# Kernel optimization log

Measured on AMD Instinct MI355X. Metric: run time of the kernel, lower is better.

## Reference

```python
import jax, jax.numpy as jnp
import numpy as np

OUT, IN, GS = 16384, 4096, 16
G = OUT * IN // GS  # 4194304 groups


def setup_inputs() -> dict:
    key = jax.random.key(0)
    k1, k2, k3, k4 = jax.random.split(key, 4)
    x = jax.random.normal(k1, (8, 32, IN), dtype=jnp.float32)
    weight_q2 = jax.random.randint(k2, (G, GS // 4), 0, 256, dtype=jnp.int32)
    weight_norm = jax.random.uniform(k3, (G, 1), dtype=jnp.float16)
    bias = jax.random.normal(k4, (OUT,), dtype=jnp.float32)
    return {"x": x, "weight_q2": weight_q2, "weight_norm": weight_norm, "bias": bias}


def _dequant_2bit(weight_q2, weight_norm):
    # torch: xq_out[:, i::4] = (xq >> 2i) & 3  =>  element index within group = i + 4*k
    # where k = packed column (slow, stride 4), i = shift index (fast).
    norm = weight_norm.astype(jnp.float32)                      # [G, 1]
    shifts = jnp.arange(4, dtype=jnp.int32) * 2                 # [4]
    vals = (weight_q2[:, :, None] >> shifts) & 3                # [G, 4(pack k), 4(shift i)]
    xq_out = vals.astype(jnp.float32).reshape(G, GS)            # [G, 16], layout k*4 + i
    w = (xq_out / 3.0) * (2.0 * norm) - norm                    # [G, 16]
    return w.reshape(OUT, IN)


def reference(x, weight_q2, weight_norm, bias):
    w = _dequant_2bit(weight_q2, weight_norm)                   # [OUT, IN] fp32
    return jnp.einsum('bsi,oi->bso', x, w) + bias
```

## Files before the change

### kernel.cpp

```cpp
#include <hip/hip_runtime.h>
#include <stdint.h>

#define M_DIM 256
#define N_DIM 16384
#define K_DIM 4096
#define BN 64
#define BK 64
#define NT (K_DIM / BK)

typedef __bf16 bf16x8 __attribute__((ext_vector_type(8)));
typedef float  f32x4  __attribute__((ext_vector_type(4)));

__device__ __forceinline__ uint32_t f2bf(float f) {
  uint32_t u = __float_as_uint(f);
  return (u + 0x7fffu + ((u >> 16) & 1u)) >> 16;
}

#define LDS_BARRIER() \
  asm volatile("s_waitcnt lgkmcnt(0)\n\ts_barrier" ::: "memory")

__global__ __launch_bounds__(256) void cvt_x_kernel(const float* __restrict__ x,
                                                    uint4* __restrict__ ws) {
  int T = blockIdx.x * 256 + threadIdx.x;
  int mb_glob = T >> 13;
  int r       = T & 8191;
  int kch     = r >> 6;
  int L       = r & 63;
  int row = mb_glob * 16 + (L & 15);
  int k   = kch * 32 + (L >> 4) * 8;
  const float* p = x + (size_t)row * K_DIM + k;
  float4 a = *(const float4*)p;
  float4 b = *(const float4*)(p + 4);
  uint4 o;
  o.x = f2bf(a.x) | (f2bf(a.y) << 16);
  o.y = f2bf(a.z) | (f2bf(a.w) << 16);
  o.z = f2bf(b.x) | (f2bf(b.y) << 16);
  o.w = f2bf(b.z) | (f2bf(b.w) << 16);
  ws[T] = o;
}

__device__ __forceinline__ uint4 deq8(uint2 q, float nv) {
  float a2 = nv * (2.0f / 3.0f);
  uint32_t tlo = f2bf(-nv) | (f2bf(fmaf(1.0f, a2, -nv)) << 16);
  uint32_t thi = f2bf(fmaf(2.0f, a2, -nv)) | (f2bf(fmaf(3.0f, a2, -nv)) << 16);
  uint32_t s0 = ((q.x & 3u) | ((q.x & 0xCu) << 14)) * 0x0202u + 0x01000100u;
  uint32_t s1 = (((q.x >> 4) & 3u) | ((q.x & 0xC0u) << 10)) * 0x0202u + 0x01000100u;
  uint32_t s2 = ((q.y & 3u) | ((q.y & 0xCu) << 14)) * 0x0202u + 0x01000100u;
  uint32_t s3 = (((q.y >> 4) & 3u) | ((q.y & 0xC0u) << 10)) * 0x0202u + 0x01000100u;
  uint4 r;
  r.x = __builtin_amdgcn_perm(thi, tlo, s0);
  r.y = __builtin_amdgcn_perm(thi, tlo, s1);
  r.z = __builtin_amdgcn_perm(thi, tlo, s2);
  r.w = __builtin_amdgcn_perm(thi, tlo, s3);
  return r;
}

__global__ __launch_bounds__(512, 4) void gemm2bit_kernel(
    const uint4*    __restrict__ aws,
    const uint32_t* __restrict__ q2,
    const float*    __restrict__ nrm,
    const float*    __restrict__ bias,
    float*          __restrict__ out)
{
  __shared__ uint4 Bb[2][512];

  const int tid  = threadIdx.x;
  const int lane = tid & 63;
  const int w    = tid >> 6;
  const int wm   = w >> 1;
  const int wn   = w & 1;
  const int lo4  = lane & 15;
  const int qd   = lane >> 4;
  const int n0   = blockIdx.x * BN;
  const int m0   = blockIdx.y * 128;

  const int lrs = lane ^ qd;

  const int nloc = tid >> 3;
  const int kg   = (tid >> 1) & 3;
  const int h    = tid & 1;
  const int grow = n0 + nloc;
  const int qd2   = (kg & 1) * 2 + h;
  const int bslot = ((kg >> 1) * 4 + (nloc >> 4)) * 64 + qd2 * 16 +
                    ((nloc & 15) ^ qd2);

  const uint4* pA = aws + ((size_t)(blockIdx.y * 8 + wm * 2) * 128) * 64 + lane;
  const uint32_t* pq = q2 + ((size_t)grow * 256 + kg) * 4 + h * 2;
  const float*    pn = nrm + (size_t)grow * 256 + kg;

  f32x4 acc[2][2];
#pragma unroll
  for (int s = 0; s < 2; ++s)
#pragma unroll
    for (int u = 0; u < 2; ++u)
      acc[s][u] = (f32x4){0.f, 0.f, 0.f, 0.f};

  uint4 af0[4], af1[4];
  uint2 qA, qB;
  float nA, nB;

#pragma unroll
  for (int s = 0; s < 2; ++s)
#pragma unroll
    for (int ts = 0; ts < 2; ++ts)
      af0[s * 2 + ts] = pA[(size_t)s * 8192 + ts * 64];
  uint2 q0 = *(const uint2*)pq;
  float n0v = pn[0];
  qA = *(const uint2*)(pq + 16);
  nA = pn[4];
  qB = *(const uint2*)(pq + 32);
  nB = pn[8];
  Bb[0][bslot] = deq8(q0, n0v);
  LDS_BARRIER();

#define GEMM_BODY(T, PR, AFC, AFN, QC, NC)                                      \
  do {                                                                          \
    if ((T) + 1 < NT) {                                                         \
      size_t toff = (size_t)((T) + 1) * 128;                                    \
      _Pragma("unroll")                                                         \
      for (int s = 0; s < 2; ++s)                                               \
        _Pragma("unroll")                                                       \
        for (int ts = 0; ts < 2; ++ts)                                          \
          AFN[s * 2 + ts] = pA[(size_t)s * 8192 + toff + ts * 64];              \
    }                                                                           \
    _Pragma("unroll")                                                           \
    for (int ts = 0; ts < 2; ++ts) {                                            \
      bf16x8 bfv[2];                                                            \
      _Pragma("unroll")                                                         \
      for (int u = 0; u < 2; ++u)                                               \
        bfv[u] = *(const bf16x8*)&Bb[PR][(ts * 4 + wn * 2 + u) * 64 + lrs];     \
      _Pragma("unroll")                                                         \
      for (int s = 0; s < 2; ++s) {                                             \
        bf16x8 av = __builtin_bit_cast(bf16x8, AFC[s * 2 + ts]);                \
        _Pragma("unroll")                                                       \
        for (int u = 0; u < 2; ++u)                                             \
          acc[s][u] = __builtin_amdgcn_mfma_f32_16x16x32_bf16(av, bfv[u],       \
                                                              acc[s][u], 0, 0, 0);\
      }                                                                         \
    }                                                                           \
    if ((T) + 1 < NT) Bb[(PR) ^ 1][bslot] = deq8(QC, NC);                       \
    if ((T) + 3 < NT) {                                                         \
      QC = *(const uint2*)(pq + (size_t)((T) + 3) * 16);                        \
      NC = pn[(size_t)((T) + 3) * 4];                                           \
    }                                                                           \
    LDS_BARRIER();                                                              \
  } while (0)

  for (int t2 = 0; t2 < NT; t2 += 2) {
    GEMM_BODY(t2,     0, af0, af1, qA, nA);
    GEMM_BODY(t2 + 1, 1, af1, af0, qB, nB);
  }
#undef GEMM_BODY

  float bv[2];
#pragma unroll
  for (int u = 0; u < 2; ++u)
    bv[u] = bias[n0 + wn * 32 + u * 16 + lo4];

#pragma unroll
  for (int s = 0; s < 2; ++s) {
    int mrow = m0 + wm * 32 + s * 16 + qd * 4;
#pragma unroll
    for (int u = 0; u < 2; ++u) {
      int ncol = n0 + wn * 32 + u * 16 + lo4;
      float* p = out + (size_t)mrow * N_DIM + ncol;
#pragma unroll
      for (int r = 0; r < 4; ++r)
        p[(size_t)r * N_DIM] = acc[s][u][r] + bv[u];
    }
  }
}

extern "C" void kernel_launch(void* const* d_in, const int* in_sizes, int n_in,
                              void* d_out, int out_size, void* d_ws, size_t ws_size,
                              hipStream_t stream) {
  const float*    x    = (const float*)d_in[0];
  const uint32_t* q2   = (const uint32_t*)d_in[1];
  const float*    nm   = (const float*)d_in[2];
  const float*    bias = (const float*)d_in[3];
  float*          out  = (float*)d_out;
  uint4*          aws  = (uint4*)d_ws;

  cvt_x_kernel<<<512, 256, 0, stream>>>(x, aws);
  gemm2bit_kernel<<<dim3(N_DIM / BN, 2), 512, 0, stream>>>(aws, q2, nm, bias, out);
}
```

Measured before the change: 166.7 us.

## Retile 2-bit GEMM to BN=32, BK=128 with 256-thread blocks

Measured after the change: 176.1 us. 1.06x slower.

```diff
diff --git a/kernel.cpp b/kernel.cpp
--- a/kernel.cpp
+++ b/kernel.cpp
@@ -4,9 +4,10 @@
 #define M_DIM 256
 #define N_DIM 16384
 #define K_DIM 4096
-#define BN 64
-#define BK 64
-#define NT (K_DIM / BK)
+#define BN 32
+#define BM 128
+#define BK 128
+#define NT2 (K_DIM / BK)
 
 typedef __bf16 bf16x8 __attribute__((ext_vector_type(8)));
 typedef float  f32x4  __attribute__((ext_vector_type(4)));
@@ -55,7 +56,7 @@
   return r;
 }
 
-__global__ __launch_bounds__(512, 4) void gemm2bit_kernel(
+__global__ __launch_bounds__(256, 4) void gemm2bit_kernel(
     const uint4*    __restrict__ aws,
     const uint32_t* __restrict__ q2,
     const float*    __restrict__ nrm,
@@ -67,12 +68,10 @@
   const int tid  = threadIdx.x;
   const int lane = tid & 63;
   const int w    = tid >> 6;
-  const int wm   = w >> 1;
-  const int wn   = w & 1;
   const int lo4  = lane & 15;
   const int qd   = lane >> 4;
   const int n0   = blockIdx.x * BN;
-  const int m0   = blockIdx.y * 128;
+  const int m0   = blockIdx.y * BM;
 
   const int lrs = lane ^ qd;
 
@@ -80,11 +79,12 @@
   const int kg   = (tid >> 1) & 3;
   const int h    = tid & 1;
   const int grow = n0 + nloc;
-  const int qd2   = (kg & 1) * 2 + h;
-  const int bslot = ((kg >> 1) * 4 + (nloc >> 4)) * 64 + qd2 * 16 +
-                    ((nloc & 15) ^ qd2);
+  const int qd2  = (kg & 1) * 2 + h;
+  const int swz  = (nloc & 15) ^ qd2;
+  const int bs0 = ((kg >> 1) * 2 + (nloc >> 4)) * 64 + qd2 * 16 + swz;
+  const int bs1 = ((2 + (kg >> 1)) * 2 + (nloc >> 4)) * 64 + qd2 * 16 + swz;
 
-  const uint4* pA = aws + ((size_t)(blockIdx.y * 8 + wm * 2) * 128) * 64 + lane;
+  const uint4* pA = aws + (size_t)(blockIdx.y * 8 + w * 2) * 8192 + lane;
   const uint32_t* pq = q2 + ((size_t)grow * 256 + kg) * 4 + h * 2;
   const float*    pn = nrm + (size_t)grow * 256 + kg;
 
@@ -95,74 +95,84 @@
     for (int u = 0; u < 2; ++u)
       acc[s][u] = (f32x4){0.f, 0.f, 0.f, 0.f};
 
-  uint4 af0[4], af1[4];
-  uint2 qA, qB;
-  float nA, nB;
+  uint4 af0[8], af1[8];
+  uint2 qa0, qa1, qb0, qb1;
+  float na0, na1, nb0, nb1;
 
 #pragma unroll
   for (int s = 0; s < 2; ++s)
 #pragma unroll
-    for (int ts = 0; ts < 2; ++ts)
-      af0[s * 2 + ts] = pA[(size_t)s * 8192 + ts * 64];
-  uint2 q0 = *(const uint2*)pq;
-  float n0v = pn[0];
-  qA = *(const uint2*)(pq + 16);
-  nA = pn[4];
-  qB = *(const uint2*)(pq + 32);
-  nB = pn[8];
-  Bb[0][bslot] = deq8(q0, n0v);
+    for (int c = 0; c < 4; ++c)
+      af0[s * 4 + c] = pA[s * 8192 + c * 64];
+  {
+    uint2 x0 = *(const uint2*)pq;
+    uint2 x1 = *(const uint2*)(pq + 16);
+    float y0 = pn[0], y1 = pn[4];
+    qa0 = *(const uint2*)(pq + 32);  qa1 = *(const uint2*)(pq + 48);
+    na0 = pn[8];  na1 = pn[12];
+    qb0 = *(const uint2*)(pq + 64);  qb1 = *(const uint2*)(pq + 80);
+    nb0 = pn[16]; nb1 = pn[20];
+    Bb[0][bs0] = deq8(x0, y0);
+    Bb[0][bs1] = deq8(x1, y1);
+  }
   LDS_BARRIER();
+  const uint4* pAp = pA + 256;
 
-#define GEMM_BODY(T, PR, AFC, AFN, QC, NC)                                      \
+#define GEMM_BODY(T, PR, AFC, AFN, Q0, Q1, N0v, N1v)                            \
   do {                                                                          \
-    if ((T) + 1 < NT) {                                                         \
-      size_t toff = (size_t)((T) + 1) * 128;                                    \
+    if ((T) + 1 < NT2) {                                                        \
       _Pragma("unroll")                                                         \
       for (int s = 0; s < 2; ++s)                                               \
         _Pragma("unroll")                                                       \
-        for (int ts = 0; ts < 2; ++ts)                                          \
-          AFN[s * 2 + ts] = pA[(size_t)s * 8192 + toff + ts * 64];              \
+        for (int c = 0; c < 4; ++c)                                             \
+          AFN[s * 4 + c] = pAp[s * 8192 + c * 64];                              \
     }                                                                           \
     _Pragma("unroll")                                                           \
-    for (int ts = 0; ts < 2; ++ts) {                                            \
+    for (int c = 0; c < 4; ++c) {                                               \
       bf16x8 bfv[2];                                                            \
       _Pragma("unroll")                                                         \
       for (int u = 0; u < 2; ++u)                                               \
-        bfv[u] = *(const bf16x8*)&Bb[PR][(ts * 4 + wn * 2 + u) * 64 + lrs];     \
+        bfv[u] = *(const bf16x8*)&Bb[PR][(c * 2 + u) * 64 + lrs];               \
       _Pragma("unroll")                                                         \
       for (int s = 0; s < 2; ++s) {                                             \
-        bf16x8 av = __builtin_bit_cast(bf16x8, AFC[s * 2 + ts]);                \
+        bf16x8 av = __builtin_bit_cast(bf16x8, AFC[s * 4 + c]);                 \
         _Pragma("unroll")                                                       \
         for (int u = 0; u < 2; ++u)                                             \
           acc[s][u] = __builtin_amdgcn_mfma_f32_16x16x32_bf16(av, bfv[u],       \
                                                               acc[s][u], 0, 0, 0);\
       }                                                                         \
     }                                                                           \
-    if ((T) + 1 < NT) Bb[(PR) ^ 1][bslot] = deq8(QC, NC);                       \
-    if ((T) + 3 < NT) {                                                         \
-      QC = *(const uint2*)(pq + (size_t)((T) + 3) * 16);                        \
-      NC = pn[(size_t)((T) + 3) * 4];                                           \
+    if ((T) + 1 < NT2) {                                                        \
+      Bb[(PR) ^ 1][bs0] = deq8(Q0, N0v);                                        \
+      Bb[(PR) ^ 1][bs1] = deq8(Q1, N1v);                                        \
     }                                                                           \
+    if ((T) + 3 < NT2) {                                                        \
+      Q0  = *(const uint2*)(pq + (size_t)((T) + 3) * 32);                       \
+      Q1  = *(const uint2*)(pq + (size_t)((T) + 3) * 32 + 16);                  \
+      N0v = pn[(size_t)((T) + 3) * 8];                                          \
+      N1v = pn[(size_t)((T) + 3) * 8 + 4];                                      \
+    }                                                                           \
+    pAp += 256;                                                                 \
     LDS_BARRIER();                                                              \
   } while (0)
 
-  for (int t2 = 0; t2 < NT; t2 += 2) {
-    GEMM_BODY(t2,     0, af0, af1, qA, nA);
-    GEMM_BODY(t2 + 1, 1, af1, af0, qB, nB);
+  for (int t2 = 0; t2 < NT2; t2 += 2) {
+    GEMM_BODY(t2,     0, af0, af1, qa0, qa1, na0, na1);
+    GEMM_BODY(t2 + 1, 1, af1, af0, qb0, qb1, nb0, nb1);
   }
 #undef GEMM_BODY
 
   float bv[2];
 #pragma unroll
   for (int u = 0; u < 2; ++u)
-    bv[u] = bias[n0 + wn * 32 + u * 16 + lo4];
+    bv[u] = bias[n0 + u * 16 + lo4];
 
 #pragma unroll
   for (int s = 0; s < 2; ++s) {
-    int mrow = m0 + wm * 32 + s * 16 + qd * 4;
+    int mrow = m0 + w * 32 + s * 16 + qd * 4;
 #pragma unroll
     for (int u = 0; u < 2; ++u) {
-      int ncol = n0 + wn * 32 + u * 16 + lo4;
+      int ncol = n0 + u * 16 + lo4;
       float* p = out + (size_t)mrow * N_DIM + ncol;
 #pragma unroll
       for (int r = 0; r < 4; ++r)
@@ -182,5 +192,5 @@
   uint4*          aws  = (uint4*)d_ws;
 
   cvt_x_kernel<<<512, 256, 0, stream>>>(x, aws);
-  gemm2bit_kernel<<<dim3(N_DIM / BN, 2), 512, 0, stream>>>(aws, q2, nm, bias, out);
+  gemm2bit_kernel<<<dim3(N_DIM / BN, 2), 256, 0, stream>>>(aws, q2, nm, bias, out);
 }
```

## Split K across two blocks with atomic accumulation and bias prefill

Applied to the files above, without the earlier changes.

Result: slower. 254.8 us (+52.8%).

```diff
diff --git a/kernel.cpp b/kernel.cpp
--- a/kernel.cpp
+++ b/kernel.cpp
@@ -6,7 +6,7 @@
 #define K_DIM 4096
 #define BN 64
 #define BK 64
-#define NT (K_DIM / BK)
+#define NTK 32
 
 typedef __bf16 bf16x8 __attribute__((ext_vector_type(8)));
 typedef float  f32x4  __attribute__((ext_vector_type(4)));
@@ -20,7 +20,9 @@
   asm volatile("s_waitcnt lgkmcnt(0)\n\ts_barrier" ::: "memory")
 
 __global__ __launch_bounds__(256) void cvt_x_kernel(const float* __restrict__ x,
-                                                    uint4* __restrict__ ws) {
+                                                    uint4* __restrict__ ws,
+                                                    const float* __restrict__ bias,
+                                                    float* __restrict__ out) {
   int T = blockIdx.x * 256 + threadIdx.x;
   int mb_glob = T >> 13;
   int r       = T & 8191;
@@ -37,6 +39,12 @@
   o.z = f2bf(b.x) | (f2bf(b.y) << 16);
   o.w = f2bf(b.z) | (f2bf(b.w) << 16);
   ws[T] = o;
+
+  const float4* b4 = (const float4*)bias;
+  float4*       o4 = (float4*)out;
+#pragma unroll
+  for (int i = T; i < (M_DIM * N_DIM / 4); i += 131072)
+    o4[i] = b4[i & 4095];
 }
 
 __device__ __forceinline__ uint4 deq8(uint2 q, float nv) {
@@ -55,11 +63,10 @@
   return r;
 }
 
-__global__ __launch_bounds__(512, 4) void gemm2bit_kernel(
+__global__ __launch_bounds__(512, 8) void gemm2bit_kernel(
     const uint4*    __restrict__ aws,
     const uint32_t* __restrict__ q2,
     const float*    __restrict__ nrm,
-    const float*    __restrict__ bias,
     float*          __restrict__ out)
 {
   __shared__ uint4 Bb[2][512];
@@ -73,6 +80,7 @@
   const int qd   = lane >> 4;
   const int n0   = blockIdx.x * BN;
   const int m0   = blockIdx.y * 128;
+  const int kz   = blockIdx.z;
 
   const int lrs = lane ^ qd;
 
@@ -84,9 +92,10 @@
   const int bslot = ((kg >> 1) * 4 + (nloc >> 4)) * 64 + qd2 * 16 +
                     ((nloc & 15) ^ qd2);
 
-  const uint4* pA = aws + ((size_t)(blockIdx.y * 8 + wm * 2) * 128) * 64 + lane;
-  const uint32_t* pq = q2 + ((size_t)grow * 256 + kg) * 4 + h * 2;
-  const float*    pn = nrm + (size_t)grow * 256 + kg;
+  const uint4* pA = aws + (size_t)(blockIdx.y * 8 + wm * 2) * 8192 +
+                    (size_t)kz * 4096 + lane;
+  const uint32_t* pq = q2 + ((size_t)grow * 256 + kz * 128 + kg) * 4 + h * 2;
+  const float*    pn = nrm + (size_t)grow * 256 + kz * 128 + kg;
 
   f32x4 acc[2][2];
 #pragma unroll
@@ -115,7 +124,7 @@
 
 #define GEMM_BODY(T, PR, AFC, AFN, QC, NC)                                      \
   do {                                                                          \
-    if ((T) + 1 < NT) {                                                         \
+    if ((T) + 1 < NTK) {                                                        \
       size_t toff = (size_t)((T) + 1) * 128;                                    \
       _Pragma("unroll")                                                         \
       for (int s = 0; s < 2; ++s)                                               \
@@ -138,24 +147,19 @@
                                                               acc[s][u], 0, 0, 0);\
       }                                                                         \
     }                                                                           \
-    if ((T) + 1 < NT) Bb[(PR) ^ 1][bslot] = deq8(QC, NC);                       \
-    if ((T) + 3 < NT) {                                                         \
+    if ((T) + 1 < NTK) Bb[(PR) ^ 1][bslot] = deq8(QC, NC);                      \
+    if ((T) + 3 < NTK) {                                                        \
       QC = *(const uint2*)(pq + (size_t)((T) + 3) * 16);                        \
       NC = pn[(size_t)((T) + 3) * 4];                                           \
     }                                                                           \
     LDS_BARRIER();                                                              \
   } while (0)
 
-  for (int t2 = 0; t2 < NT; t2 += 2) {
+  for (int t2 = 0; t2 < NTK; t2 += 2) {
     GEMM_BODY(t2,     0, af0, af1, qA, nA);
     GEMM_BODY(t2 + 1, 1, af1, af0, qB, nB);
   }
 #undef GEMM_BODY
-
-  float bv[2];
-#pragma unroll
-  for (int u = 0; u < 2; ++u)
-    bv[u] = bias[n0 + wn * 32 + u * 16 + lo4];
 
 #pragma unroll
   for (int s = 0; s < 2; ++s) {
@@ -166,7 +170,7 @@
       float* p = out + (size_t)mrow * N_DIM + ncol;
 #pragma unroll
       for (int r = 0; r < 4; ++r)
-        p[(size_t)r * N_DIM] = acc[s][u][r] + bv[u];
+        atomicAdd(p + (size_t)r * N_DIM, acc[s][u][r]);
     }
   }
 }
@@ -181,6 +185,6 @@
   float*          out  = (float*)d_out;
   uint4*          aws  = (uint4*)d_ws;
 
-  cvt_x_kernel<<<512, 256, 0, stream>>>(x, aws);
-  gemm2bit_kernel<<<dim3(N_DIM / BN, 2), 512, 0, stream>>>(aws, q2, nm, bias, out);
+  cvt_x_kernel<<<512, 256, 0, stream>>>(x, aws, bias, out);
+  gemm2bit_kernel<<<dim3(N_DIM / BN, 2, 2), 512, 0, stream>>>(aws, q2, nm, out);
 }
```

## Fuse fp32-to-bf16 activation conversion into the GEMM main loop

Applied to the files above, without the earlier changes.

Result: slower. 338.5 us (+103.0%).

```diff
diff --git a/kernel.cpp b/kernel.cpp
--- a/kernel.cpp
+++ b/kernel.cpp
@@ -16,28 +16,17 @@
   return (u + 0x7fffu + ((u >> 16) & 1u)) >> 16;
 }
 
-#define LDS_BARRIER() \
-  asm volatile("s_waitcnt lgkmcnt(0)\n\ts_barrier" ::: "memory")
-
-__global__ __launch_bounds__(256) void cvt_x_kernel(const float* __restrict__ x,
-                                                    uint4* __restrict__ ws) {
-  int T = blockIdx.x * 256 + threadIdx.x;
-  int mb_glob = T >> 13;
-  int r       = T & 8191;
-  int kch     = r >> 6;
-  int L       = r & 63;
-  int row = mb_glob * 16 + (L & 15);
-  int k   = kch * 32 + (L >> 4) * 8;
-  const float* p = x + (size_t)row * K_DIM + k;
-  float4 a = *(const float4*)p;
-  float4 b = *(const float4*)(p + 4);
+__device__ __forceinline__ uint4 packbf8(float4 a, float4 b) {
   uint4 o;
   o.x = f2bf(a.x) | (f2bf(a.y) << 16);
   o.y = f2bf(a.z) | (f2bf(a.w) << 16);
   o.z = f2bf(b.x) | (f2bf(b.y) << 16);
   o.w = f2bf(b.z) | (f2bf(b.w) << 16);
-  ws[T] = o;
+  return o;
 }
+
+#define LDS_BARRIER() \
+  asm volatile("s_waitcnt lgkmcnt(0)\n\ts_barrier" ::: "memory")
 
 __device__ __forceinline__ uint4 deq8(uint2 q, float nv) {
   float a2 = nv * (2.0f / 3.0f);
@@ -56,7 +45,7 @@
 }
 
 __global__ __launch_bounds__(512, 4) void gemm2bit_kernel(
-    const uint4*    __restrict__ aws,
+    const float*    __restrict__ x,
     const uint32_t* __restrict__ q2,
     const float*    __restrict__ nrm,
     const float*    __restrict__ bias,
@@ -84,7 +73,8 @@
   const int bslot = ((kg >> 1) * 4 + (nloc >> 4)) * 64 + qd2 * 16 +
                     ((nloc & 15) ^ qd2);
 
-  const uint4* pA = aws + ((size_t)(blockIdx.y * 8 + wm * 2) * 128) * 64 + lane;
+  const float* pX0 = x + (size_t)(m0 + (wm * 2 + 0) * 16 + lo4) * K_DIM + qd * 8;
+  const float* pX1 = x + (size_t)(m0 + (wm * 2 + 1) * 16 + lo4) * K_DIM + qd * 8;
   const uint32_t* pq = q2 + ((size_t)grow * 256 + kg) * 4 + h * 2;
   const float*    pn = nrm + (size_t)grow * 256 + kg;
 
@@ -95,15 +85,21 @@
     for (int u = 0; u < 2; ++u)
       acc[s][u] = (f32x4){0.f, 0.f, 0.f, 0.f};
 
-  uint4 af0[4], af1[4];
+  float4 raw[4][2];
+  uint4  apkE[4], apkO[4];
   uint2 qA, qB;
   float nA, nB;
 
 #pragma unroll
-  for (int s = 0; s < 2; ++s)
+  for (int s = 0; s < 2; ++s) {
+    const float* px = s ? pX1 : pX0;
 #pragma unroll
-    for (int ts = 0; ts < 2; ++ts)
-      af0[s * 2 + ts] = pA[(size_t)s * 8192 + ts * 64];
+    for (int ts = 0; ts < 2; ++ts) {
+      float4 f0 = *(const float4*)(px + ts * 32);
+      float4 f1 = *(const float4*)(px + ts * 32 + 4);
+      apkE[s * 2 + ts] = packbf8(f0, f1);
+    }
+  }
   uint2 q0 = *(const uint2*)pq;
   float n0v = pn[0];
   qA = *(const uint2*)(pq + 16);
@@ -113,15 +109,19 @@
   Bb[0][bslot] = deq8(q0, n0v);
   LDS_BARRIER();
 
-#define GEMM_BODY(T, PR, AFC, AFN, QC, NC)                                      \
+#define GEMM_BODY(T, PR, APK, APKN, QC, NC)                                     \
   do {                                                                          \
     if ((T) + 1 < NT) {                                                         \
-      size_t toff = (size_t)((T) + 1) * 128;                                    \
       _Pragma("unroll")                                                         \
-      for (int s = 0; s < 2; ++s)                                               \
+      for (int s = 0; s < 2; ++s) {                                             \
+        const float* px = s ? pX1 : pX0;                                        \
         _Pragma("unroll")                                                       \
-        for (int ts = 0; ts < 2; ++ts)                                          \
-          AFN[s * 2 + ts] = pA[(size_t)s * 8192 + toff + ts * 64];              \
+        for (int ts = 0; ts < 2; ++ts) {                                        \
+          raw[s * 2 + ts][0] = *(const float4*)(px + ((T) + 1) * 64 + ts * 32); \
+          raw[s * 2 + ts][1] =                                                  \
+              *(const float4*)(px + ((T) + 1) * 64 + ts * 32 + 4);              \
+        }                                                                       \
+      }                                                                         \
     }                                                                           \
     _Pragma("unroll")                                                           \
     for (int ts = 0; ts < 2; ++ts) {                                            \
@@ -131,7 +131,7 @@
         bfv[u] = *(const bf16x8*)&Bb[PR][(ts * 4 + wn * 2 + u) * 64 + lrs];     \
       _Pragma("unroll")                                                         \
       for (int s = 0; s < 2; ++s) {                                             \
-        bf16x8 av = __builtin_bit_cast(bf16x8, AFC[s * 2 + ts]);                \
+        bf16x8 av = __builtin_bit_cast(bf16x8, APK[s * 2 + ts]);                \
         _Pragma("unroll")                                                       \
         for (int u = 0; u < 2; ++u)                                             \
           acc[s][u] = __builtin_amdgcn_mfma_f32_16x16x32_bf16(av, bfv[u],       \
@@ -143,12 +143,16 @@
       QC = *(const uint2*)(pq + (size_t)((T) + 3) * 16);                        \
       NC = pn[(size_t)((T) + 3) * 4];                                           \
     }                                                                           \
+    if ((T) + 1 < NT) {                                                         \
+      _Pragma("unroll")                                                         \
+      for (int j = 0; j < 4; ++j) APKN[j] = packbf8(raw[j][0], raw[j][1]);      \
+    }                                                                           \
     LDS_BARRIER();                                                              \
   } while (0)
 
   for (int t2 = 0; t2 < NT; t2 += 2) {
-    GEMM_BODY(t2,     0, af0, af1, qA, nA);
-    GEMM_BODY(t2 + 1, 1, af1, af0, qB, nB);
+    GEMM_BODY(t2,     0, apkE, apkO, qA, nA);
+    GEMM_BODY(t2 + 1, 1, apkO, apkE, qB, nB);
   }
 #undef GEMM_BODY
 
@@ -179,8 +183,7 @@
   const float*    nm   = (const float*)d_in[2];
   const float*    bias = (const float*)d_in[3];
   float*          out  = (float*)d_out;
-  uint4*          aws  = (uint4*)d_ws;
+  (void)d_ws; (void)ws_size;
 
-  cvt_x_kernel<<<512, 256, 0, stream>>>(x, aws);
-  gemm2bit_kernel<<<dim3(N_DIM / BN, 2), 512, 0, stream>>>(aws, q2, nm, bias, out);
+  gemm2bit_kernel<<<dim3(N_DIM / BN, 2), 512, 0, stream>>>(x, q2, nm, bias, out);
 }
```
